# Kernel tuning notes

Hardware: AMD Instinct MI355X
Metric: run time of the kernel (lower is better)

Reference implementation:

```python
import jax, jax.numpy as jnp
import numpy as np

B, P_LEN, Q_LEN, HID = 8, 2048, 1024, 1024


def setup_inputs() -> dict:
    key = jax.random.key(0)
    k1, k2, k3, k4 = jax.random.split(key, 4)
    k = jax.random.normal(k1, (B, P_LEN, HID), dtype=jnp.float32)
    q = jax.random.normal(k2, (B, Q_LEN, HID), dtype=jnp.float32)
    # q_mask: True = pad token. All-valid mask (no pads) to avoid NaN rows.
    q_mask = jnp.zeros((B, Q_LEN), dtype=bool)
    # Xavier-normal-initialized Linear weights, shape [out, in] as in torch.
    std = float(np.sqrt(2.0 / (HID + HID)))
    Wk = jax.random.normal(k3, (HID, HID), dtype=jnp.float32) * std
    Wq = jax.random.normal(k4, (HID, HID), dtype=jnp.float32) * std
    return {"k": k, "q": q, "q_mask": q_mask, "Wk": Wk, "Wq": Wq}


def reference(k, q, q_mask, Wk, Wq):
    # relu-projected keys/queries (Linear has no bias)
    p_key = jax.nn.relu(jnp.einsum('bpd,hd->bph', k, Wk))   # [B, p_len, hid]
    q_key = jax.nn.relu(jnp.einsum('bqd,hd->bqh', q, Wq))   # [B, q_len, hid]
    scores = jnp.einsum('bph,bqh->bpq', p_key, q_key)        # [B, p_len, q_len]
    scores = jnp.where(q_mask[:, None, :], -jnp.inf, scores)
    alphas = jax.nn.softmax(scores, axis=-1)                 # [B, p_len, q_len]
    ctx = jnp.einsum('bpq,bqd->bpd', alphas, q)              # [B, p_len, q_dim]
    return ctx, alphas
```

## Files before the change

### kernel.cpp

```cpp
#include <hip/hip_runtime.h>
#include <hip/hip_bf16.h>
#include <math.h>


typedef _Float16 v8h __attribute__((ext_vector_type(8)));
typedef _Float16 v4h __attribute__((ext_vector_type(4)));
typedef float v4f __attribute__((ext_vector_type(4)));

#define AS1C(p) ((const __attribute__((address_space(1))) void*)(p))
#define AS3(p)  ((__attribute__((address_space(3))) void*)(p))

__global__ __launch_bounds__(256) void gemm_nt_f16(
    const _Float16* __restrict__ A, const _Float16* __restrict__ B,
    float* __restrict__ Cf, _Float16* __restrict__ Ch,
    int N, int K, int Mtiles, int Ntiles,
    long long sA, long long sB, long long sC, int relu)
{
  __shared__ _Float16 As[128 * 32];
  __shared__ _Float16 Bs[128 * 32];

  const int bid = blockIdx.x;
  const int mt  = bid % Mtiles;
  const int nt  = (bid / Mtiles) % Ntiles;
  const int bz  = bid / (Mtiles * Ntiles);

  A += (long long)bz * sA;
  B += (long long)bz * sB;

  const int m0 = mt * 128;
  const int n0 = nt * 128;
  const int t  = threadIdx.x;
  const int l  = t & 63;
  const int w  = t >> 6;
  const int wm = (w >> 1) * 64;
  const int wn = (w & 1) * 64;
  const int fr = l & 15;
  const int fq = l >> 4;

  const int srow = t >> 2;
  const int scol = (t & 3) << 3;

  v4f acc[4][4];
#pragma unroll
  for (int i = 0; i < 4; ++i)
#pragma unroll
    for (int j = 0; j < 4; ++j)
      acc[i][j] = (v4f){0.f, 0.f, 0.f, 0.f};

  const _Float16* Ap = A + (long long)(m0 + srow) * K + scol;
  const _Float16* Bp = B + (long long)(n0 + srow) * K + scol;

  for (int k0 = 0; k0 < K; k0 += 32) {
    __builtin_amdgcn_global_load_lds(AS1C(Ap + k0),          AS3(As + t * 8),        16, 0, 0);
    __builtin_amdgcn_global_load_lds(AS1C(Ap + 64 * K + k0), AS3(As + 2048 + t * 8), 16, 0, 0);
    __builtin_amdgcn_global_load_lds(AS1C(Bp + k0),          AS3(Bs + t * 8),        16, 0, 0);
    __builtin_amdgcn_global_load_lds(AS1C(Bp + 64 * K + k0), AS3(Bs + 2048 + t * 8), 16, 0, 0);
    __syncthreads();

    v8h a[4], b[4];
#pragma unroll
    for (int i = 0; i < 4; ++i)
      a[i] = *(const v8h*)&As[(wm + i * 16 + fr) * 32 + fq * 8];
#pragma unroll
    for (int j = 0; j < 4; ++j)
      b[j] = *(const v8h*)&Bs[(wn + j * 16 + fr) * 32 + fq * 8];

#pragma unroll
    for (int i = 0; i < 4; ++i)
#pragma unroll
      for (int j = 0; j < 4; ++j)
        acc[i][j] = __builtin_amdgcn_mfma_f32_16x16x32_f16(a[i], b[j], acc[i][j], 0, 0, 0);

    __syncthreads();
  }

  float* Cfb = Cf ? Cf + (long long)bz * sC : nullptr;
  _Float16* Chb = Ch ? Ch + (long long)bz * sC : nullptr;
#pragma unroll
  for (int i = 0; i < 4; ++i) {
#pragma unroll
    for (int j = 0; j < 4; ++j) {
#pragma unroll
      for (int r = 0; r < 4; ++r) {
        const int row = m0 + wm + i * 16 + fq * 4 + r;
        const int col = n0 + wn + j * 16 + fr;
        float v = acc[i][j][r];
        if (relu) v = fmaxf(v, 0.f);
        if (Cfb) Cfb[(long long)row * N + col] = v;
        if (Chb) Chb[(long long)row * N + col] = (_Float16)v;
      }
    }
  }
}

__global__ __launch_bounds__(256) void convert_all_kernel(
    const float* __restrict__ s0, _Float16* __restrict__ d0, int b0,
    const float* __restrict__ s1, _Float16* __restrict__ d1, int b1,
    const float* __restrict__ s2, _Float16* __restrict__ d2, int b2,
    const float* __restrict__ s3, _Float16* __restrict__ d3)
{
  int blk = blockIdx.x;
  const float* src;
  _Float16* dst;
  if (blk < b0)           { src = s0; dst = d0; }
  else if (blk < b0 + b1) { src = s1; dst = d1; blk -= b0; }
  else if (blk < b0 + b1 + b2) { src = s2; dst = d2; blk -= b0 + b1; }
  else                    { src = s3; dst = d3; blk -= b0 + b1 + b2; }
  const long long i = ((long long)blk * 256 + threadIdx.x) * 4;
  const float4 v = *(const float4*)(src + i);
  v4h o = {(_Float16)v.x, (_Float16)v.y, (_Float16)v.z, (_Float16)v.w};
  *(v4h*)(dst + i) = o;
}

__global__ __launch_bounds__(256) void transpose_f16_kernel(
    const float* __restrict__ q, _Float16* __restrict__ qT, int Q, int H)
{
  __shared__ float tile[64][65];
  const float* qb = q + (long long)blockIdx.z * Q * H;
  _Float16* qTb = qT + (long long)blockIdx.z * H * Q;
  const int q0 = blockIdx.x * 64, h0 = blockIdx.y * 64;
  const int t = threadIdx.x;
  const int tr = t >> 4, tc = (t & 15) << 2;
#pragma unroll
  for (int i = 0; i < 4; ++i) {
    const float4 v = *(const float4*)(qb + (long long)(q0 + tr + i * 16) * H + h0 + tc);
    tile[tr + i * 16][tc + 0] = v.x;
    tile[tr + i * 16][tc + 1] = v.y;
    tile[tr + i * 16][tc + 2] = v.z;
    tile[tr + i * 16][tc + 3] = v.w;
  }
  __syncthreads();
#pragma unroll
  for (int i = 0; i < 4; ++i) {
    const int hl = tr + i * 16;
    const int ql = tc;
    v4h o = {(_Float16)tile[ql + 0][hl], (_Float16)tile[ql + 1][hl],
             (_Float16)tile[ql + 2][hl], (_Float16)tile[ql + 3][hl]};
    *(v4h*)(qTb + (long long)(h0 + hl) * Q + q0 + ql) = o;
  }
}

__global__ __launch_bounds__(256) void softmax_rows_kernel(
    float* __restrict__ S, _Float16* __restrict__ S16,
    const unsigned char* __restrict__ qmask, int Q, int P)
{
  const long long row = blockIdx.x;
  const int b = (int)(row / P);
  float* s = S + row * (long long)Q;
  const unsigned char* msk = qmask + (long long)b * Q;
  const int t = threadIdx.x;
  float4 v = *(const float4*)(s + (t << 2));
  float vals[4] = {v.x, v.y, v.z, v.w};
#pragma unroll
  for (int j = 0; j < 4; ++j)
    if (msk[(t << 2) + j]) vals[j] = -INFINITY;

  __shared__ float red[8];
  const int wid = t >> 6, lid = t & 63;

  float mx = fmaxf(fmaxf(vals[0], vals[1]), fmaxf(vals[2], vals[3]));
#pragma unroll
  for (int o = 32; o > 0; o >>= 1) mx = fmaxf(mx, __shfl_xor(mx, o, 64));
  if (lid == 0) red[wid] = mx;
  __syncthreads();
  mx = fmaxf(fmaxf(red[0], red[1]), fmaxf(red[2], red[3]));

  float e[4];
  float sum = 0.f;
#pragma unroll
  for (int j = 0; j < 4; ++j) { e[j] = __expf(vals[j] - mx); sum += e[j]; }
#pragma unroll
  for (int o = 32; o > 0; o >>= 1) sum += __shfl_xor(sum, o, 64);
  __syncthreads();
  if (lid == 0) red[4 + wid] = sum;
  __syncthreads();
  sum = red[4] + red[5] + red[6] + red[7];
  const float inv = 1.f / sum;

  float4 o;
  o.x = e[0] * inv; o.y = e[1] * inv; o.z = e[2] * inv; o.w = e[3] * inv;
  *(float4*)(s + (t << 2)) = o;
  v4h oh = {(_Float16)o.x, (_Float16)o.y, (_Float16)o.z, (_Float16)o.w};
  *(v4h*)(S16 + row * (long long)Q + (t << 2)) = oh;
}

extern "C" void kernel_launch(void* const* d_in, const int* in_sizes, int n_in,
                              void* d_out, int out_size, void* d_ws, size_t ws_size,
                              hipStream_t stream)
{
  const int B = 8, P = 2048, Q = 1024, H = 1024;
  const float* k  = (const float*)d_in[0];
  const float* q  = (const float*)d_in[1];
  const unsigned char* qmask = (const unsigned char*)d_in[2];
  const float* Wk = (const float*)d_in[3];
  const float* Wq = (const float*)d_in[4];

  float* ctx    = (float*)d_out;
  float* alphas = ctx + (size_t)B * P * H;

  _Float16* pkey16 = (_Float16*)d_out;

  char* wsb = (char*)d_ws;
  _Float16* qkey16   = (_Float16*)(wsb);
  _Float16* k16      = (_Float16*)(wsb + 16777216);
  _Float16* alphas16 = k16;
  _Float16* q16      = (_Float16*)(wsb + 16777216 + 33554432);
  _Float16* qT16     = q16;
  _Float16* Wk16     = (_Float16*)(wsb + 67108864);
  _Float16* Wq16     = (_Float16*)(wsb + 69206016);

  const long long nK = (long long)B * P * H;
  const long long nQ = (long long)B * Q * H;
  const long long nW = (long long)H * H;

  const int bK = (int)(nK / 1024), bQ = (int)(nQ / 1024), bW = (int)(nW / 1024);
  convert_all_kernel<<<bK + bQ + 2 * bW, 256, 0, stream>>>(
      k, k16, bK, q, q16, bQ, Wk, Wk16, bW, Wq, Wq16);

  gemm_nt_f16<<<(16384 / 128) * (1024 / 128), 256, 0, stream>>>(
      k16, Wk16, nullptr, pkey16, H, H, 16384 / 128, 1024 / 128, 0LL, 0LL, 0LL, 1);
  gemm_nt_f16<<<(8192 / 128) * (1024 / 128), 256, 0, stream>>>(
      q16, Wq16, nullptr, qkey16, H, H, 8192 / 128, 1024 / 128, 0LL, 0LL, 0LL, 1);
  gemm_nt_f16<<<(P / 128) * (Q / 128) * B, 256, 0, stream>>>(
      pkey16, qkey16, alphas, nullptr, Q, H, P / 128, Q / 128,
      (long long)P * H, (long long)Q * H, (long long)P * Q, 0);
  transpose_f16_kernel<<<dim3(Q / 64, H / 64, B), 256, 0, stream>>>(q, qT16, Q, H);
  softmax_rows_kernel<<<B * P, 256, 0, stream>>>(alphas, alphas16, qmask, Q, P);
  gemm_nt_f16<<<(P / 128) * (H / 128) * B, 256, 0, stream>>>(
      alphas16, qT16, ctx, nullptr, H, Q, P / 128, H / 128,
      (long long)P * Q, (long long)H * Q, (long long)P * H, 0);
}
```

Measured before the change: 441.3 us.

## Use 256x256 GEMM tiles with 4-stage LDS pipeline and XCD-aware block remap

Replaces the 128x128 single-buffered GEMM with a 512-thread 256x256 tile kernel. It uses a 4-deep ring of LDS stages fed by async global_load_lds, with vmcnt waits so loads overlap MFMA work. Block indices are remapped so consecutive tiles land on the same XCD for L2 reuse, and setprio raises MFMA priority. It needs 128KB of dynamic LDS, which allows only one block per CU, and the grids are small: 128 blocks for the q projection and 256 for the others.

```diff
diff --git a/kernel.cpp b/kernel.cpp
--- a/kernel.cpp
+++ b/kernel.cpp
@@ -10,16 +10,17 @@
 #define AS1C(p) ((const __attribute__((address_space(1))) void*)(p))
 #define AS3(p)  ((__attribute__((address_space(3))) void*)(p))
 
-__global__ __launch_bounds__(256) void gemm_nt_f16(
+__global__ __launch_bounds__(512) void gemm_nt_f16_256(
     const _Float16* __restrict__ A, const _Float16* __restrict__ B,
     float* __restrict__ Cf, _Float16* __restrict__ Ch,
     int N, int K, int Mtiles, int Ntiles,
     long long sA, long long sB, long long sC, int relu)
 {
-  __shared__ _Float16 As[128 * 32];
-  __shared__ _Float16 Bs[128 * 32];
-
-  const int bid = blockIdx.x;
+  extern __shared__ _Float16 lds[];
+
+  const int nwg = gridDim.x;
+  const int cpx = nwg >> 3;
+  const int bid = (blockIdx.x & 7) * cpx + (blockIdx.x >> 3);
   const int mt  = bid % Mtiles;
   const int nt  = (bid / Mtiles) % Ntiles;
   const int bz  = bid / (Mtiles * Ntiles);
@@ -27,57 +28,83 @@
   A += (long long)bz * sA;
   B += (long long)bz * sB;
 
-  const int m0 = mt * 128;
-  const int n0 = nt * 128;
+  const int m0 = mt * 256;
+  const int n0 = nt * 256;
   const int t  = threadIdx.x;
   const int l  = t & 63;
   const int w  = t >> 6;
-  const int wm = (w >> 1) * 64;
-  const int wn = (w & 1) * 64;
+  const int wm = (w >> 2) * 128;
+  const int wn = (w & 3) * 64;
   const int fr = l & 15;
   const int fq = l >> 4;
 
-  const int srow = t >> 2;
-  const int scol = (t & 3) << 3;
-
-  v4f acc[4][4];
-#pragma unroll
-  for (int i = 0; i < 4; ++i)
+  const int tr = t >> 2;
+  const int tc = (t & 3) * 8;
+
+  const _Float16* A0 = A + (long long)(m0 + tr) * K + tc;
+  const _Float16* A1 = A + (long long)(m0 + 128 + tr) * K + tc;
+  const _Float16* B0 = B + (long long)(n0 + tr) * K + tc;
+  const _Float16* B1 = B + (long long)(n0 + 128 + tr) * K + tc;
+
+  v4f acc[8][4];
+#pragma unroll
+  for (int i = 0; i < 8; ++i)
 #pragma unroll
     for (int j = 0; j < 4; ++j)
       acc[i][j] = (v4f){0.f, 0.f, 0.f, 0.f};
 
-  const _Float16* Ap = A + (long long)(m0 + srow) * K + scol;
-  const _Float16* Bp = B + (long long)(n0 + srow) * K + scol;
-
-  for (int k0 = 0; k0 < K; k0 += 32) {
-    __builtin_amdgcn_global_load_lds(AS1C(Ap + k0),          AS3(As + t * 8),        16, 0, 0);
-    __builtin_amdgcn_global_load_lds(AS1C(Ap + 64 * K + k0), AS3(As + 2048 + t * 8), 16, 0, 0);
-    __builtin_amdgcn_global_load_lds(AS1C(Bp + k0),          AS3(Bs + t * 8),        16, 0, 0);
-    __builtin_amdgcn_global_load_lds(AS1C(Bp + 64 * K + k0), AS3(Bs + 2048 + t * 8), 16, 0, 0);
-    __syncthreads();
-
-    v8h a[4], b[4];
-#pragma unroll
-    for (int i = 0; i < 4; ++i)
-      a[i] = *(const v8h*)&As[(wm + i * 16 + fr) * 32 + fq * 8];
+  const int NT = K >> 5;
+
+#define STAGE(kt) do {                                                              \
+    _Float16* s_ = lds + (((kt) & 3) << 14);                                        \
+    const int ko_ = (kt) << 5;                                                      \
+    __builtin_amdgcn_global_load_lds(AS1C(A0 + ko_), AS3(s_ +         t * 8), 16, 0, 0); \
+    __builtin_amdgcn_global_load_lds(AS1C(A1 + ko_), AS3(s_ +  4096 + t * 8), 16, 0, 0); \
+    __builtin_amdgcn_global_load_lds(AS1C(B0 + ko_), AS3(s_ +  8192 + t * 8), 16, 0, 0); \
+    __builtin_amdgcn_global_load_lds(AS1C(B1 + ko_), AS3(s_ + 12288 + t * 8), 16, 0, 0); \
+  } while (0)
+
+  STAGE(0);
+  STAGE(1);
+  STAGE(2);
+
+  for (int kt = 0; kt < NT; ++kt) {
+    if (kt < NT - 2)       asm volatile("s_waitcnt vmcnt(8)" ::: "memory");
+    else if (kt == NT - 2) asm volatile("s_waitcnt vmcnt(4)" ::: "memory");
+    else                   asm volatile("s_waitcnt vmcnt(0)" ::: "memory");
+    __builtin_amdgcn_sched_barrier(0);
+    __builtin_amdgcn_s_barrier();
+    asm volatile("" ::: "memory");
+
+    if (kt + 3 < NT) STAGE(kt + 3);
+
+    const _Float16* As_ = lds + ((kt & 3) << 14);
+    const _Float16* Bs_ = As_ + 8192;
+
+    v8h a[8], b[4];
+#pragma unroll
+    for (int i = 0; i < 8; ++i)
+      a[i] = *(const v8h*)&As_[(wm + i * 16 + fr) * 32 + fq * 8];
 #pragma unroll
     for (int j = 0; j < 4; ++j)
-      b[j] = *(const v8h*)&Bs[(wn + j * 16 + fr) * 32 + fq * 8];
-
-#pragma unroll
-    for (int i = 0; i < 4; ++i)
+      b[j] = *(const v8h*)&Bs_[(wn + j * 16 + fr) * 32 + fq * 8];
+
+    __builtin_amdgcn_s_setprio(1);
+#pragma unroll
+    for (int i = 0; i < 8; ++i)
 #pragma unroll
       for (int j = 0; j < 4; ++j)
         acc[i][j] = __builtin_amdgcn_mfma_f32_16x16x32_f16(a[i], b[j], acc[i][j], 0, 0, 0);
-
-    __syncthreads();
-  }
+    __builtin_amdgcn_s_setprio(0);
+    asm volatile("s_waitcnt lgkmcnt(0)" ::: "memory");
+    __builtin_amdgcn_sched_barrier(0);
+  }
+#undef STAGE
 
   float* Cfb = Cf ? Cf + (long long)bz * sC : nullptr;
   _Float16* Chb = Ch ? Ch + (long long)bz * sC : nullptr;
 #pragma unroll
-  for (int i = 0; i < 4; ++i) {
+  for (int i = 0; i < 8; ++i) {
 #pragma unroll
     for (int j = 0; j < 4; ++j) {
 #pragma unroll
@@ -217,16 +244,17 @@
   convert_all_kernel<<<bK + bQ + 2 * bW, 256, 0, stream>>>(
       k, k16, bK, q, q16, bQ, Wk, Wk16, bW, Wq, Wq16);
 
-  gemm_nt_f16<<<(16384 / 128) * (1024 / 128), 256, 0, stream>>>(
-      k16, Wk16, nullptr, pkey16, H, H, 16384 / 128, 1024 / 128, 0LL, 0LL, 0LL, 1);
-  gemm_nt_f16<<<(8192 / 128) * (1024 / 128), 256, 0, stream>>>(
-      q16, Wq16, nullptr, qkey16, H, H, 8192 / 128, 1024 / 128, 0LL, 0LL, 0LL, 1);
-  gemm_nt_f16<<<(P / 128) * (Q / 128) * B, 256, 0, stream>>>(
-      pkey16, qkey16, alphas, nullptr, Q, H, P / 128, Q / 128,
+  const size_t LDSB = 131072;
+  gemm_nt_f16_256<<<64 * 4, 512, LDSB, stream>>>(
+      k16, Wk16, nullptr, pkey16, H, H, 64, 4, 0LL, 0LL, 0LL, 1);
+  gemm_nt_f16_256<<<32 * 4, 512, LDSB, stream>>>(
+      q16, Wq16, nullptr, qkey16, H, H, 32, 4, 0LL, 0LL, 0LL, 1);
+  gemm_nt_f16_256<<<8 * 4 * B, 512, LDSB, stream>>>(
+      pkey16, qkey16, alphas, nullptr, Q, H, 8, 4,
       (long long)P * H, (long long)Q * H, (long long)P * Q, 0);
   transpose_f16_kernel<<<dim3(Q / 64, H / 64, B), 256, 0, stream>>>(q, qT16, Q, H);
   softmax_rows_kernel<<<B * P, 256, 0, stream>>>(alphas, alphas16, qmask, Q, P);
-  gemm_nt_f16<<<(P / 128) * (H / 128) * B, 256, 0, stream>>>(
-      alphas16, qT16, ctx, nullptr, H, Q, P / 128, H / 128,
+  gemm_nt_f16_256<<<8 * 4 * B, 512, LDSB, stream>>>(
+      alphas16, qT16, ctx, nullptr, H, Q, 8, 4,
       (long long)P * Q, (long long)H * Q, (long long)P * H, 0);
 }
```

New measurement: 394.9 us. 10.5% less time.
